# Kernel optimization log

Hardware: AMD Instinct MI355X
Metric: run time of the kernel (lower is better)

The kernel has to match this reference:

```python
import jax, jax.numpy as jnp
import numpy as np

DIM = 512
NUM_LATENTS = 512
HIDDEN = 48  # PointEmbed sinusoidal embedding dim (divisible by 6)


def make_basis():
    k = HIDDEN // 6
    e = (2.0 ** np.arange(k)) * np.pi
    z = np.zeros(k)
    basis = np.stack([
        np.concatenate([e, z, z]),
        np.concatenate([z, e, z]),
        np.concatenate([z, z, e]),
    ])  # [3, HIDDEN//2]
    return jnp.asarray(basis, jnp.float32)


def layernorm(x, g, b, eps=1e-5):
    m = x.mean(-1, keepdims=True)
    v = ((x - m) ** 2).mean(-1, keepdims=True)
    return (x - m) / jnp.sqrt(v + eps) * g + b


def point_embed(x, basis, w, b):
    # x: [B, N, 3] -> [B, N, DIM//2]
    proj = jnp.einsum('bnd,de->bne', x, basis)
    feat = jnp.concatenate([jnp.sin(proj), jnp.cos(proj), x], axis=-1)  # [B,N,51]
    return feat @ w + b


def fps_single(points, num_samples):
    # deterministic farthest point sampling starting at index 0; non-differentiable
    pts = jax.lax.stop_gradient(points)
    N = pts.shape[0]

    def body(carry, _):
        dists, last = carry
        d = jnp.sum((pts - pts[last]) ** 2, axis=-1)
        dists = jnp.minimum(dists, d)
        nxt = jnp.argmax(dists).astype(jnp.int32)
        return (dists, nxt), nxt

    init = (jnp.full((N,), 1e10, pts.dtype), jnp.int32(0))
    _, idxs = jax.lax.scan(body, init, None, length=num_samples - 1)
    return jnp.concatenate([jnp.zeros((1,), jnp.int32), idxs])


def setup_inputs() -> dict:
    key = jax.random.key(0)
    ks = jax.random.split(key, 16)
    B, T, N, D = 16, 3, 2048, 3
    s = 0.02
    inp = {
        'pc': jax.random.normal(ks[0], (B, T, N, D), jnp.float32),
        'pc2': jax.random.normal(ks[1], (B, T, N, D), jnp.float32),
        'basis': make_basis(),
        'pe_w': jax.random.normal(ks[2], (HIDDEN + 3, DIM // 2), jnp.float32) * s,
        'pe_b': jnp.zeros((DIM // 2,), jnp.float32),
        'lnq_g': jnp.ones((DIM,), jnp.float32), 'lnq_b': jnp.zeros((DIM,), jnp.float32),
        'lnc_g': jnp.ones((DIM,), jnp.float32), 'lnc_b': jnp.zeros((DIM,), jnp.float32),
        'wq': jax.random.normal(ks[3], (DIM, DIM), jnp.float32) * s,
        'wkv': jax.random.normal(ks[4], (DIM, 2 * DIM), jnp.float32) * s,
        'wo': jax.random.normal(ks[5], (DIM, DIM), jnp.float32) * s,
        'bo': jnp.zeros((DIM,), jnp.float32),
        'lnf_g': jnp.ones((DIM,), jnp.float32), 'lnf_b': jnp.zeros((DIM,), jnp.float32),
        'w1': jax.random.normal(ks[6], (DIM, 8 * DIM), jnp.float32) * s,
        'b1': jnp.zeros((8 * DIM,), jnp.float32),
        'w2': jax.random.normal(ks[7], (4 * DIM, DIM), jnp.float32) * s,
        'b2': jnp.zeros((DIM,), jnp.float32),
    }
    return inp


def reference(pc, pc2, basis, pe_w, pe_b, lnq_g, lnq_b, lnc_g, lnc_b,
              wq, wkv, wo, bo, lnf_g, lnf_b, w1, b1, w2, b2):
    B, T, N, D = pc.shape
    # FPS on the first frame, per batch element (batch-local indices)
    idx = jax.vmap(lambda p: fps_single(p, NUM_LATENTS))(pc[:, 0])  # [B, M]
    idx4 = idx[:, None, :, None]  # broadcast over T and D
    sampled = jnp.take_along_axis(pc, idx4, axis=2).reshape(B * T, NUM_LATENTS, D)
    sampled2 = jnp.take_along_axis(pc2, idx4, axis=2).reshape(B * T, NUM_LATENTS, D)
    pcf = pc.reshape(B * T, N, D)
    pcf2 = pc2.reshape(B * T, N, D)

    emb_s = jnp.concatenate([point_embed(sampled, basis, pe_w, pe_b),
                             point_embed(sampled2, basis, pe_w, pe_b)], axis=-1)
    emb_c = jnp.concatenate([point_embed(pcf, basis, pe_w, pe_b),
                             point_embed(pcf2, basis, pe_w, pe_b)], axis=-1)

    # PreNorm cross-attention (1 head, dim_head = DIM)
    q_in = layernorm(emb_s, lnq_g, lnq_b)
    c_in = layernorm(emb_c, lnc_g, lnc_b)
    q = q_in @ wq
    kv = c_in @ wkv
    k, v = jnp.split(kv, 2, axis=-1)
    scale = DIM ** -0.5
    attn = jax.nn.softmax(jnp.einsum('bmd,bnd->bmn', q, k) * scale, axis=-1)
    out = jnp.einsum('bmn,bnd->bmd', attn, v) @ wo + bo
    x = out + emb_s

    # PreNorm GEGLU feed-forward
    h = layernorm(x, lnf_g, lnf_b) @ w1 + b1
    a, g = jnp.split(h, 2, axis=-1)
    x = (a * jax.nn.gelu(g, approximate=False)) @ w2 + b2 + x

    return x.reshape(B, T, NUM_LATENTS, DIM)
```

## Files before the change

### kernel.cpp

```cpp
#include <hip/hip_runtime.h>

#define NB    16
#define NT    3
#define NCTX  2048
#define NLAT  512
#define DIMV  512
#define HALFD 256
#define NFEAT 51
#define NBT   48
#define MROWS 24576
#define GRP   6
#define NGRP  8
#define GROWS 12288
#define FUSED_BLKS (NB + GROWS/16 + 4096)

typedef unsigned short bfu;
typedef short bf16x8 __attribute__((ext_vector_type(8)));
typedef float f32x4  __attribute__((ext_vector_type(4)));
typedef float f32x2  __attribute__((ext_vector_type(2)));

__device__ __forceinline__ float bf2f(bfu u){ return __uint_as_float(((unsigned int)u) << 16); }
__device__ __forceinline__ bfu f2bf(float f){
  unsigned int u = __float_as_uint(f);
  u += 0x7FFFu + ((u >> 16) & 1u);
  return (bfu)(u >> 16);
}
__device__ __forceinline__ float loadE(const float* p){ return *p; }
__device__ __forceinline__ float loadE(const bfu* p){ return bf2f(*p); }
__device__ __forceinline__ void storeE(float* p, float v){ *p = v; }
__device__ __forceinline__ void storeE(bfu* p, float v){ *p = f2bf(v); }
__device__ __forceinline__ bfu to_bfu(float f){ return f2bf(f); }
__device__ __forceinline__ bfu to_bfu(bfu u){ return u; }

#define GLD16(gp, lp) __builtin_amdgcn_global_load_lds(                       \
    (const __attribute__((address_space(1))) unsigned int*)(gp),              \
    (__attribute__((address_space(3))) unsigned int*)(lp), 16, 0, 0)

template<int KSTEP>
__device__ __forceinline__ int swzr(int r){
  constexpr int CPR = KSTEP / 8;
  return (KSTEP == 32) ? ((r >> 1) & 3) : (r & (CPR - 1));
}

#define DPP_ARGMAX_STAGE(CTRL)                                                \
  {                                                                           \
    const int svb = __builtin_amdgcn_update_dpp(vb, vb, CTRL, 0xF, 0xF, false); \
    const int sib = __builtin_amdgcn_update_dpp(ib, ib, CTRL, 0xF, 0xF, false); \
    const float sv = __int_as_float(svb);                                     \
    const float cv = __int_as_float(vb);                                      \
    if (sv > cv || (sv == cv && sib < ib)){ vb = svb; ib = sib; }             \
  }

__device__ __forceinline__ void fps_body(int b, int tid, const float* __restrict__ pc,
                                         int* __restrict__ idx_out,
                                         float4* pts, int (*mbuf)[8]){
  const int lane = tid & 63, w = tid >> 6;
  const int wbase = w << 9;
  const float* src = pc + (size_t)b * (NT * NCTX * 3);

  f32x2 x2[4], y2[4], z2[4], d2[4];
  #pragma unroll
  for (int j = 0; j < 4; ++j){
    #pragma unroll
    for (int h = 0; h < 2; ++h){
      const int p = wbase + ((2 * j + h) << 6) + lane;
      const float xx = src[p * 3 + 0];
      const float yy = src[p * 3 + 1];
      const float zz = src[p * 3 + 2];
      x2[j][h] = xx; y2[j][h] = yy; z2[j][h] = zz;
      pts[p] = make_float4(xx, yy, zz, 0.f);
    }
    d2[j][0] = 1e10f; d2[j][1] = 1e10f;
  }
  if (tid == 0) idx_out[b * NLAT] = 0;
  __syncthreads();

  int last = 0;
  for (int step = 1; step < NLAT; ++step){
    const float4 lp = pts[last];

    #pragma unroll
    for (int j = 0; j < 4; ++j){
      const f32x2 dx = x2[j] - lp.x;
      const f32x2 dy = y2[j] - lp.y;
      const f32x2 dz = z2[j] - lp.z;
      const f32x2 dd = (dx * dx + dy * dy) + dz * dz;
      f32x2 nd;
      nd[0] = fminf(d2[j][0], dd[0]);
      nd[1] = fminf(d2[j][1], dd[1]);
      d2[j] = nd;
    }

    float av[4]; int as_[4];
    #pragma unroll
    for (int j = 0; j < 4; ++j){
      const float lo = d2[j][0], hi = d2[j][1];
      const bool t = hi > lo;
      av[j]  = t ? hi : lo;
      as_[j] = t ? 2 * j + 1 : 2 * j;
    }
    #pragma unroll
    for (int wdt = 2; wdt; wdt >>= 1){
      #pragma unroll
      for (int j = 0; j < wdt; ++j){
        const float lv = av[2 * j], rv = av[2 * j + 1];
        const int   li = as_[2 * j], ri = as_[2 * j + 1];
        const bool t = rv > lv;
        av[j]  = t ? rv : lv;
        as_[j] = t ? ri : li;
      }
    }

    int vb = __float_as_int(av[0]);
    int ib = wbase + (as_[0] << 6) + lane;
    DPP_ARGMAX_STAGE(0x111)
    DPP_ARGMAX_STAGE(0x112)
    DPP_ARGMAX_STAGE(0x114)
    DPP_ARGMAX_STAGE(0x118)
    DPP_ARGMAX_STAGE(0x142)
    DPP_ARGMAX_STAGE(0x143)

    const int par = step & 1;
    if (lane == 63){ mbuf[par][w * 2] = vb; mbuf[par][w * 2 + 1] = ib; }
    __syncthreads();
    const int4 q0 = *(const int4*)&mbuf[par][0];
    const int4 q1 = *(const int4*)&mbuf[par][4];
    float bv = __int_as_float(q0.x); int bi = q0.y;
    { const float v1 = __int_as_float(q0.z); if (v1 > bv){ bv = v1; bi = q0.w; } }
    { const float v2 = __int_as_float(q1.x); if (v2 > bv){ bv = v2; bi = q1.y; } }
    { const float v3 = __int_as_float(q1.z); if (v3 > bv){ bv = v3; bi = q1.w; } }
    last = bi;
    if (tid == 0) idx_out[b * NLAT + step] = last;
  }
}

template<bool GATHER, bool WRITE_EMB>
__device__ __forceinline__ void embed_body(
    int bid, int tid,
    const float* __restrict__ pc, const float* __restrict__ pc2,
    const int* __restrict__ idx,
    const float* __restrict__ basis, const float* __restrict__ pe_w,
    const float* __restrict__ pe_b,
    const float* __restrict__ ln_g, const float* __restrict__ ln_b,
    bfu* __restrict__ emb, bfu* __restrict__ lnout, int nppbt,
    float (*feat)[16][NFEAT + 1], float (*outb)[DIMV])
{
  const int p0 = bid << 4;

  if (tid < 32){
    const int s = tid >> 4, p = tid & 15;
    const int gp = p0 + p;
    const int bt = gp / nppbt;
    const int n  = gp - bt * nppbt;
    const int bb = bt / NT;
    const int srcn = GATHER ? idx[bb * NLAT + n] : n;
    const float* sp = (s ? pc2 : pc) + ((size_t)bt * NCTX + srcn) * 3;
    feat[s][p][48] = sp[0]; feat[s][p][49] = sp[1]; feat[s][p][50] = sp[2];
  }
  __syncthreads();

  #pragma unroll
  for (int t = 0; t < 3; ++t){
    const int wk  = tid * 3 + t;
    const int spq = wk / 24;
    const int e   = wk - spq * 24;
    const int s = spq >> 4, p = spq & 15;
    const float x0 = feat[s][p][48], x1 = feat[s][p][49], x2 = feat[s][p][50];
    const float pr = __fadd_rn(__fadd_rn(__fmul_rn(x0, basis[e]),
                                         __fmul_rn(x1, basis[24 + e])),
                               __fmul_rn(x2, basis[48 + e]));
    feat[s][p][e]      = sinf(pr);
    feat[s][p][24 + e] = cosf(pr);
  }
  __syncthreads();

  {
    float w[NFEAT];
    #pragma unroll
    for (int k = 0; k < NFEAT; ++k) w[k] = pe_w[k * HALFD + tid];
    const float bv = pe_b[tid];
    #pragma unroll
    for (int half = 0; half < 2; ++half){
      for (int p = 0; p < 16; ++p){
        float acc = bv;
        #pragma unroll
        for (int k = 0; k < NFEAT; ++k) acc = fmaf(feat[half][p][k], w[k], acc);
        outb[p][half * HALFD + tid] = acc;
      }
    }
  }
  __syncthreads();

  const int lane = tid & 63, wv = tid >> 6;
  for (int pp = 0; pp < 4; ++pp){
    const int p = (wv << 2) + pp;
    const size_t gp = (size_t)p0 + p;
    float x[8];
    #pragma unroll
    for (int j = 0; j < 8; ++j) x[j] = outb[p][lane + (j << 6)];
    float s = 0.f;
    #pragma unroll
    for (int j = 0; j < 8; ++j) s += x[j];
    for (int o = 32; o; o >>= 1) s += __shfl_xor(s, o, 64);
    const float m = s * (1.0f / 512.0f);
    float s2 = 0.f;
    #pragma unroll
    for (int j = 0; j < 8; ++j){ const float d = x[j] - m; s2 = fmaf(d, d, s2); }
    for (int o = 32; o; o >>= 1) s2 += __shfl_xor(s2, o, 64);
    const float inv = 1.0f / sqrtf(s2 * (1.0f / 512.0f) + 1e-5f);
    #pragma unroll
    for (int j = 0; j < 8; ++j){
      const int c = lane + (j << 6);
      const float r = (x[j] - m) * inv * ln_g[c] + ln_b[c];
      const size_t o2 = gp * DIMV + c;
      if (WRITE_EMB) emb[o2] = f2bf(x[j]);
      lnout[o2] = f2bf(r);
    }
  }
}

template<bool GATHER, bool WRITE_EMB>
__global__ __launch_bounds__(256) void embed_kernel(
    const float* __restrict__ pc, const float* __restrict__ pc2,
    const int* __restrict__ idx,
    const float* __restrict__ basis, const float* __restrict__ pe_w,
    const float* __restrict__ pe_b,
    const float* __restrict__ ln_g, const float* __restrict__ ln_b,
    bfu* __restrict__ emb, bfu* __restrict__ lnout, int nppbt)
{
  __shared__ float feat[2][16][NFEAT + 1];
  __shared__ float outb[16][DIMV];
  embed_body<GATHER, WRITE_EMB>(blockIdx.x, threadIdx.x, pc, pc2, idx, basis,
      pe_w, pe_b, ln_g, ln_b, emb, lnout, nppbt, feat, outb);
}

template<typename TIN>
__device__ __forceinline__ void transp_body(
    const TIN* __restrict__ in, bfu* __restrict__ out, int R, int C,
    int bx, int by, bfu (*t)[33])
{
  const int c0 = bx * 32, r0 = by * 32;
  const int tx = threadIdx.x & 31, ty = threadIdx.x >> 5;
  #pragma unroll
  for (int rr = ty; rr < 32; rr += 8)
    t[rr][tx] = to_bfu(in[(size_t)(r0 + rr) * C + c0 + tx]);
  __syncthreads();
  #pragma unroll
  for (int rr = ty; rr < 32; rr += 8)
    out[(size_t)(c0 + rr) * R + r0 + tx] = t[tx][rr];
}

__global__ __attribute__((amdgpu_waves_per_eu(1, 1)))
__launch_bounds__(256) void fused_pre(
    const float* __restrict__ pc, const float* __restrict__ pc2,
    int* __restrict__ idx_out,
    const float* __restrict__ basis, const float* __restrict__ pe_w,
    const float* __restrict__ pe_b,
    const float* __restrict__ lnc_g, const float* __restrict__ lnc_b,
    bfu* __restrict__ c_grp,
    const float* __restrict__ wq, const float* __restrict__ wkv,
    const float* __restrict__ wo, const float* __restrict__ w1,
    const float* __restrict__ w2,
    bfu* __restrict__ wqT, bfu* __restrict__ wkvT, bfu* __restrict__ woT,
    bfu* __restrict__ w1T, bfu* __restrict__ w2T)
{
  __shared__ __align__(16) char smem[39424];
  const int bid = blockIdx.x, tid = threadIdx.x;

  if (bid < NB){
    #pragma clang fp contract(off)
    float4* pts = (float4*)smem;
    int (*mbuf)[8] = (int(*)[8])(smem + 32768);
    fps_body(bid, tid, pc, idx_out, pts, mbuf);
    return;
  }
  const int rb = bid - NB;
  if (rb < GROWS / 16){
    embed_body<false, false>(rb, tid, pc, pc2, nullptr, basis, pe_w, pe_b,
                             lnc_g, lnc_b, nullptr, c_grp, NCTX,
                             (float(*)[16][NFEAT + 1])smem,
                             (float(*)[DIMV])(smem + 6656));
    return;
  }
  int tb = rb - GROWS / 16;
  bfu (*tile)[33] = (bfu(*)[33])smem;
  if (tb < 256){ transp_body<float>(wq,  wqT,  512,  512, tb & 15,  tb >> 4, tile); return; }
  tb -= 256;
  if (tb < 512){ transp_body<float>(wkv, wkvT, 512, 1024, tb & 31,  tb >> 5, tile); return; }
  tb -= 512;
  if (tb < 256){ transp_body<float>(wo,  woT,  512,  512, tb & 15,  tb >> 4, tile); return; }
  tb -= 256;
  if (tb < 2048){ transp_body<float>(w1, w1T,  512, 4096, tb & 127, tb >> 7, tile); return; }
  tb -= 2048;
  transp_body<float>(w2, w2T, 2048, 512, tb & 15, tb >> 4, tile);
}

#define EPI_NONE     0
#define EPI_SPLIT    1
#define EPI_SCALE    2
#define EPI_BIAS_RES 3

template<int FH, int KSTEP, typename TC, typename TR, int EPI>
__global__ __launch_bounds__(256, 2) void gemm_mfma(
    const bfu* __restrict__ A, const bfu* __restrict__ B,
    TC* __restrict__ C, TC* __restrict__ C2,
    const float* __restrict__ bias, const TR* __restrict__ res,
    float scale, int N, int K, int lda, int ldb, int ldc,
    long long sA, long long sB, long long sC)
{
  constexpr int BT  = FH * 32;
  constexpr int CPR = KSTEP / 8;
  constexpr int NI  = (BT * CPR) / 256;
  const int bz = blockIdx.z;
  A += (size_t)bz * sA;
  B += (size_t)bz * sB;
  const size_t coff = (size_t)bz * sC;

  __shared__ __align__(16) short As[BT * KSTEP];
  __shared__ __align__(16) short Bs[BT * KSTEP];

  const int tid = threadIdx.x;
  const int lane = tid & 63, w = tid >> 6;
  const int wl = (w << 6) + lane;
  const int m0 = blockIdx.y * BT, n0 = blockIdx.x * BT;
  const int wm = (w & 1) * (FH * 16), wn = (w >> 1) * (FH * 16);
  const int fr = lane & 15, quad = lane >> 4;

  f32x4 acc[FH][FH];
  #pragma unroll
  for (int i = 0; i < FH; ++i)
    #pragma unroll
    for (int j = 0; j < FH; ++j)
      #pragma unroll
      for (int r = 0; r < 4; ++r) acc[i][j][r] = 0.f;

  for (int k0 = 0; k0 < K; k0 += KSTEP){
    #pragma unroll
    for (int i = 0; i < NI; ++i){
      const int ch = i * 256 + wl;
      const int r  = ch / CPR, cs = ch & (CPR - 1);
      const int cg = cs ^ swzr<KSTEP>(r);
      short* la = (short*)As + ((i * 256 + (w << 6)) << 3);
      short* lb = (short*)Bs + ((i * 256 + (w << 6)) << 3);
      GLD16(A + (size_t)(m0 + r) * lda + k0 + cg * 8, la);
      GLD16(B + (size_t)(n0 + r) * ldb + k0 + cg * 8, lb);
    }
    __syncthreads();
    #pragma unroll
    for (int kk = 0; kk < KSTEP / 32; ++kk){
      bf16x8 af[FH], bf[FH];
      #pragma unroll
      for (int i = 0; i < FH; ++i){
        const int row = wm + i * 16 + fr;
        const int cl = (kk * 4 + quad) ^ swzr<KSTEP>(row);
        af[i] = *(const bf16x8*)&As[row * KSTEP + (cl << 3)];
      }
      #pragma unroll
      for (int j = 0; j < FH; ++j){
        const int row = wn + j * 16 + fr;
        const int cl = (kk * 4 + quad) ^ swzr<KSTEP>(row);
        bf[j] = *(const bf16x8*)&Bs[row * KSTEP + (cl << 3)];
      }
      #pragma unroll
      for (int i = 0; i < FH; ++i)
        #pragma unroll
        for (int j = 0; j < FH; ++j)
          acc[i][j] = __builtin_amdgcn_mfma_f32_16x16x32_bf16(af[i], bf[j], acc[i][j], 0, 0, 0);
    }
    __syncthreads();
  }

  TC* Cp = C + coff;
  #pragma unroll
  for (int i = 0; i < FH; ++i){
    #pragma unroll
    for (int r = 0; r < 4; ++r){
      const int cm = m0 + wm + i * 16 + quad * 4 + r;
      #pragma unroll
      for (int j = 0; j < FH; ++j){
        const int cn = n0 + wn + j * 16 + fr;
        float v = acc[i][j][r];
        if (EPI == EPI_SCALE)    v *= scale;
        if (EPI == EPI_BIAS_RES) v = v + bias[cn] + loadE(&res[coff + (size_t)cm * ldc + cn]);
        if (EPI == EPI_SPLIT){
          const int half = N >> 1;
          if (cn < half) storeE(&C [(size_t)cm * half + cn],          v);
          else           storeE(&C2[(size_t)cm * half + (cn - half)], v);
        } else {
          storeE(&Cp[(size_t)cm * ldc + cn], v);
        }
      }
    }
  }
}

__global__ __launch_bounds__(256, 1) void mlp1_mfma(
    const bfu* __restrict__ A, const bfu* __restrict__ B,
    const float* __restrict__ b1, bfu* __restrict__ act)
{
  constexpr int KSTEP = 64, CPR = 8, NI = 4;
  __shared__ __align__(16) short As[128 * KSTEP];
  __shared__ __align__(16) short Ba[128 * KSTEP];
  __shared__ __align__(16) short Bg[128 * KSTEP];

  const int tid = threadIdx.x;
  const int lane = tid & 63, w = tid >> 6;
  const int wl = (w << 6) + lane;
  const int m0 = blockIdx.y * 128, n0 = blockIdx.x * 128;
  const int wm = (w & 1) * 64, wn = (w >> 1) * 64;
  const int fr = lane & 15, quad = lane >> 4;

  f32x4 acca[4][4], accg[4][4];
  #pragma unroll
  for (int i = 0; i < 4; ++i)
    #pragma unroll
    for (int j = 0; j < 4; ++j)
      #pragma unroll
      for (int r = 0; r < 4; ++r){ acca[i][j][r] = 0.f; accg[i][j][r] = 0.f; }

  for (int k0 = 0; k0 < 512; k0 += KSTEP){
    #pragma unroll
    for (int i = 0; i < NI; ++i){
      const int ch = i * 256 + wl;
      const int r  = ch / CPR, cs = ch & (CPR - 1);
      const int cg = cs ^ swzr<KSTEP>(r);
      short* da = (short*)As + ((i * 256 + (w << 6)) << 3);
      short* db = (short*)Ba + ((i * 256 + (w << 6)) << 3);
      short* dg = (short*)Bg + ((i * 256 + (w << 6)) << 3);
      GLD16(A + (size_t)(m0 + r) * 512 + k0 + cg * 8, da);
      GLD16(B + (size_t)(n0 + r) * 512 + k0 + cg * 8, db);
      GLD16(B + (size_t)(n0 + 2048 + r) * 512 + k0 + cg * 8, dg);
    }
    __syncthreads();
    #pragma unroll
    for (int kk = 0; kk < KSTEP / 32; ++kk){
      bf16x8 af[4], ba[4], bg[4];
      #pragma unroll
      for (int i = 0; i < 4; ++i){
        const int row = wm + i * 16 + fr;
        const int cl = (kk * 4 + quad) ^ swzr<KSTEP>(row);
        af[i] = *(const bf16x8*)&As[row * KSTEP + (cl << 3)];
      }
      #pragma unroll
      for (int j = 0; j < 4; ++j){
        const int row = wn + j * 16 + fr;
        const int cl = (kk * 4 + quad) ^ swzr<KSTEP>(row);
        ba[j] = *(const bf16x8*)&Ba[row * KSTEP + (cl << 3)];
        bg[j] = *(const bf16x8*)&Bg[row * KSTEP + (cl << 3)];
      }
      #pragma unroll
      for (int i = 0; i < 4; ++i)
        #pragma unroll
        for (int j = 0; j < 4; ++j){
          acca[i][j] = __builtin_amdgcn_mfma_f32_16x16x32_bf16(af[i], ba[j], acca[i][j], 0, 0, 0);
          accg[i][j] = __builtin_amdgcn_mfma_f32_16x16x32_bf16(af[i], bg[j], accg[i][j], 0, 0, 0);
        }
    }
    __syncthreads();
  }

  #pragma unroll
  for (int i = 0; i < 4; ++i){
    #pragma unroll
    for (int r = 0; r < 4; ++r){
      const int cm = m0 + wm + i * 16 + quad * 4 + r;
      #pragma unroll
      for (int j = 0; j < 4; ++j){
        const int cn = n0 + wn + j * 16 + fr;
        const float a = acca[i][j][r] + b1[cn];
        const float g = accg[i][j][r] + b1[cn + 2048];
        const float ge = g * 0.5f * (1.0f + erff(g * 0.70710678118654752f));
        act[(size_t)cm * 2048 + cn] = f2bf(a * ge);
      }
    }
  }
}

__global__ __launch_bounds__(256) void softmax_kernel(bfu* __restrict__ sc){
  __shared__ float red[4];
  const int tid = threadIdx.x;
  const int lane = tid & 63, wv = tid >> 6;
  bfu* rp = sc + (size_t)blockIdx.x * NCTX;
  float x[8];
  #pragma unroll
  for (int j = 0; j < 8; ++j) x[j] = bf2f(rp[tid + (j << 8)]);
  float mx = x[0];
  #pragma unroll
  for (int j = 1; j < 8; ++j) mx = fmaxf(mx, x[j]);
  for (int o = 32; o; o >>= 1) mx = fmaxf(mx, __shfl_xor(mx, o, 64));
  if (lane == 0) red[wv] = mx;
  __syncthreads();
  mx = fmaxf(fmaxf(red[0], red[1]), fmaxf(red[2], red[3]));
  float sum = 0.f;
  #pragma unroll
  for (int j = 0; j < 8; ++j){ x[j] = __expf(x[j] - mx); sum += x[j]; }
  for (int o = 32; o; o >>= 1) sum += __shfl_xor(sum, o, 64);
  __syncthreads();
  if (lane == 0) red[wv] = sum;
  __syncthreads();
  sum = red[0] + red[1] + red[2] + red[3];
  const float inv = 1.0f / sum;
  #pragma unroll
  for (int j = 0; j < 8; ++j) rp[tid + (j << 8)] = f2bf(x[j] * inv);
}

__global__ __launch_bounds__(256) void ln_kernel(const float* __restrict__ in,
                                                 const float* __restrict__ g,
                                                 const float* __restrict__ b,
                                                 bfu* __restrict__ out){
  const int tid = threadIdx.x, lane = tid & 63, wv = tid >> 6;
  const size_t row = (size_t)blockIdx.x * 4 + wv;
  const float* rp = in + row * DIMV;
  float x[8];
  #pragma unroll
  for (int j = 0; j < 8; ++j) x[j] = rp[lane + (j << 6)];
  float s = 0.f;
  #pragma unroll
  for (int j = 0; j < 8; ++j) s += x[j];
  for (int o = 32; o; o >>= 1) s += __shfl_xor(s, o, 64);
  const float m = s * (1.0f / 512.0f);
  float s2 = 0.f;
  #pragma unroll
  for (int j = 0; j < 8; ++j){ const float d = x[j] - m; s2 = fmaf(d, d, s2); }
  for (int o = 32; o; o >>= 1) s2 += __shfl_xor(s2, o, 64);
  const float inv = 1.0f / sqrtf(s2 * (1.0f / 512.0f) + 1e-5f);
  bfu* op = out + row * DIMV;
  #pragma unroll
  for (int j = 0; j < 8; ++j){
    const int c = lane + (j << 6);
    op[c] = f2bf((x[j] - m) * inv * g[c] + b[c]);
  }
}

extern "C" void kernel_launch(void* const* d_in, const int* in_sizes, int n_in,
                              void* d_out, int out_size, void* d_ws, size_t ws_size,
                              hipStream_t stream)
{
  (void)in_sizes; (void)n_in; (void)out_size;
  if (ws_size < 121667584ull) return;

  const float* pc    = (const float*)d_in[0];
  const float* pc2   = (const float*)d_in[1];
  const float* basis = (const float*)d_in[2];
  const float* pe_w  = (const float*)d_in[3];
  const float* pe_b  = (const float*)d_in[4];
  const float* lnq_g = (const float*)d_in[5];
  const float* lnq_b = (const float*)d_in[6];
  const float* lnc_g = (const float*)d_in[7];
  const float* lnc_b = (const float*)d_in[8];
  const float* wq    = (const float*)d_in[9];
  const float* wkv   = (const float*)d_in[10];
  const float* wo    = (const float*)d_in[11];
  const float* bo    = (const float*)d_in[12];
  const float* lnf_g = (const float*)d_in[13];
  const float* lnf_b = (const float*)d_in[14];
  const float* w1    = (const float*)d_in[15];
  const float* b1    = (const float*)d_in[16];
  const float* w2    = (const float*)d_in[17];
  const float* b2    = (const float*)d_in[18];
  float* xout = (float*)d_out;

  char* ws = (char*)d_ws;
  int* idxb   = (int*)(ws);
  bfu* emb_s  = (bfu*)(ws + 32768);
  bfu* q_in   = (bfu*)(ws + 25198592);
  bfu* c_grp  = (bfu*)(ws + 50364416);
  bfu* k_grp  = (bfu*)(ws + 62947328);
  bfu* v_grp  = (bfu*)(ws + 75530240);
  bfu* qbuf   = (bfu*)(ws + 88113152);
  bfu* wqT    = (bfu*)(ws + 113278976);
  bfu* wkvT   = (bfu*)(ws + 113803264);
  bfu* woT    = (bfu*)(ws + 114851840);
  bfu* w1T    = (bfu*)(ws + 115376128);
  bfu* w2T    = (bfu*)(ws + 119570432);
  bfu* scores  = c_grp;
  bfu* vT      = v_grp;
  bfu* attnout = q_in;
  bfu* lnx     = qbuf;
  bfu* actb    = emb_s;

  fused_pre<<<FUSED_BLKS, 256, 0, stream>>>(
      pc, pc2, idxb, basis, pe_w, pe_b, lnc_g, lnc_b, c_grp,
      wq, wkv, wo, w1, w2, wqT, wkvT, woT, w1T, w2T);

  embed_kernel<true, true><<<MROWS/16, 256, 0, stream>>>(
      pc, pc2, idxb, basis, pe_w, pe_b, lnq_g, lnq_b, emb_s, q_in, NLAT);

  gemm_mfma<4, 64, bfu, float, EPI_NONE><<<dim3(4, 192, 1), 256, 0, stream>>>(
      q_in, wqT, qbuf, nullptr, nullptr, nullptr, 1.0f,
      512, 512, 512, 512, 512, 0, 0, 0);

  for (int g = 0; g < NGRP; ++g){
    const int bt0 = g * GRP;
    if (g > 0){
      embed_kernel<false, false><<<GROWS/16, 256, 0, stream>>>(
          pc + (size_t)bt0 * NCTX * 3, pc2 + (size_t)bt0 * NCTX * 3, nullptr,
          basis, pe_w, pe_b, lnc_g, lnc_b, nullptr, c_grp, NCTX);
    }

    gemm_mfma<4, 64, bfu, float, EPI_NONE><<<dim3(4, 96, 1), 256, 0, stream>>>(
        c_grp, wkvT, k_grp, nullptr, nullptr, nullptr, 1.0f,
        512, 512, 512, 512, 512, 0, 0, 0);

    gemm_mfma<4, 64, bfu, float, EPI_NONE><<<dim3(16, 4, GRP), 256, 0, stream>>>(
        wkvT + 512 * 512, c_grp, v_grp, nullptr, nullptr, nullptr, 1.0f,
        2048, 512, 512, 512, 2048, 0, 1048576, 1048576);

    gemm_mfma<4, 64, bfu, float, EPI_SCALE><<<dim3(16, 4, GRP), 256, 0, stream>>>(
        qbuf + (size_t)bt0 * 262144, k_grp, scores, nullptr, nullptr, nullptr,
        0.044194173824159216f,
        2048, 512, 512, 512, 2048, 262144, 1048576, 1048576);

    softmax_kernel<<<GRP * 512, 256, 0, stream>>>(scores);

    gemm_mfma<2, 128, bfu, float, EPI_NONE><<<dim3(8, 8, GRP), 256, 0, stream>>>(
        scores, vT, attnout + (size_t)bt0 * 262144, nullptr, nullptr, nullptr, 1.0f,
        512, 2048, 2048, 2048, 512, 1048576, 1048576, 262144);
  }

  gemm_mfma<4, 64, float, bfu, EPI_BIAS_RES><<<dim3(4, 192, 1), 256, 0, stream>>>(
      attnout, woT, xout, nullptr, bo, emb_s, 1.0f,
      512, 512, 512, 512, 512, 0, 0, 0);

  ln_kernel<<<MROWS/4, 256, 0, stream>>>(xout, lnf_g, lnf_b, lnx);

  for (int h = 0; h < 2; ++h){
    const size_t ro = (size_t)h * 12288;
    mlp1_mfma<<<dim3(16, 96, 1), 256, 0, stream>>>(
        lnx + ro * 512, w1T, b1, actb);
    gemm_mfma<4, 64, float, float, EPI_BIAS_RES><<<dim3(4, 96, 1), 256, 0, stream>>>(
        actb, w2T, xout + ro * 512, nullptr, b2, xout + ro * 512, 1.0f,
        512, 2048, 2048, 2048, 512, 0, 0, 0);
  }
}
```

Baseline: 1.527 ms.

## Broadcast FPS winner coordinates via LDS and merge Q/K/V GEMMs into one launch

```diff
diff --git a/kernel.cpp b/kernel.cpp
--- a/kernel.cpp
+++ b/kernel.cpp
@@ -53,7 +53,7 @@
 
 __device__ __forceinline__ void fps_body(int b, int tid, const float* __restrict__ pc,
                                          int* __restrict__ idx_out,
-                                         float4* pts, int (*mbuf)[8]){
+                                         float4 (*xyz)[4], int2 (*vi)[4]){
   const int lane = tid & 63, w = tid >> 6;
   const int wbase = w << 9;
   const float* src = pc + (size_t)b * (NT * NCTX * 3);
@@ -64,21 +64,20 @@
     #pragma unroll
     for (int h = 0; h < 2; ++h){
       const int p = wbase + ((2 * j + h) << 6) + lane;
-      const float xx = src[p * 3 + 0];
-      const float yy = src[p * 3 + 1];
-      const float zz = src[p * 3 + 2];
-      x2[j][h] = xx; y2[j][h] = yy; z2[j][h] = zz;
-      pts[p] = make_float4(xx, yy, zz, 0.f);
+      x2[j][h] = src[p * 3 + 0];
+      y2[j][h] = src[p * 3 + 1];
+      z2[j][h] = src[p * 3 + 2];
     }
     d2[j][0] = 1e10f; d2[j][1] = 1e10f;
   }
-  if (tid == 0) idx_out[b * NLAT] = 0;
+  if (tid == 0){
+    idx_out[b * NLAT] = 0;
+    xyz[0][0] = make_float4(x2[0][0], y2[0][0], z2[0][0], 0.f);
+  }
   __syncthreads();
-
-  int last = 0;
+  float4 lp = xyz[0][0];
+
   for (int step = 1; step < NLAT; ++step){
-    const float4 lp = pts[last];
-
     #pragma unroll
     for (int j = 0; j < 4; ++j){
       const f32x2 dx = x2[j] - lp.x;
@@ -121,16 +120,41 @@
     DPP_ARGMAX_STAGE(0x143)
 
     const int par = step & 1;
-    if (lane == 63){ mbuf[par][w * 2] = vb; mbuf[par][w * 2 + 1] = ib; }
+    if (lane == 63) vi[par][w] = make_int2(vb, ib);
+    if ((ib & 63) == lane){
+      const int s = (ib >> 6) & 7;
+      const bool b0 = (s & 1) != 0, b1 = (s & 2) != 0, b2 = (s & 4) != 0;
+      const float xa = b0 ? x2[0][1] : x2[0][0];
+      const float xb = b0 ? x2[1][1] : x2[1][0];
+      const float xc = b0 ? x2[2][1] : x2[2][0];
+      const float xd = b0 ? x2[3][1] : x2[3][0];
+      const float ya = b0 ? y2[0][1] : y2[0][0];
+      const float yb = b0 ? y2[1][1] : y2[1][0];
+      const float yc = b0 ? y2[2][1] : y2[2][0];
+      const float yd = b0 ? y2[3][1] : y2[3][0];
+      const float za = b0 ? z2[0][1] : z2[0][0];
+      const float zb = b0 ? z2[1][1] : z2[1][0];
+      const float zc = b0 ? z2[2][1] : z2[2][0];
+      const float zd = b0 ? z2[3][1] : z2[3][0];
+      const float xe = b1 ? xb : xa, xf = b1 ? xd : xc;
+      const float ye = b1 ? yb : ya, yf = b1 ? yd : yc;
+      const float ze = b1 ? zb : za, zf = b1 ? zd : zc;
+      xyz[par][w] = make_float4(b2 ? xf : xe, b2 ? yf : ye, b2 ? zf : ze, 0.f);
+    }
     __syncthreads();
-    const int4 q0 = *(const int4*)&mbuf[par][0];
-    const int4 q1 = *(const int4*)&mbuf[par][4];
-    float bv = __int_as_float(q0.x); int bi = q0.y;
-    { const float v1 = __int_as_float(q0.z); if (v1 > bv){ bv = v1; bi = q0.w; } }
-    { const float v2 = __int_as_float(q1.x); if (v2 > bv){ bv = v2; bi = q1.y; } }
-    { const float v3 = __int_as_float(q1.z); if (v3 > bv){ bv = v3; bi = q1.w; } }
-    last = bi;
-    if (tid == 0) idx_out[b * NLAT + step] = last;
+
+    const int2 r0 = vi[par][0], r1 = vi[par][1], r2 = vi[par][2], r3 = vi[par][3];
+    const float4 c0 = xyz[par][0], c1 = xyz[par][1], c2 = xyz[par][2], c3 = xyz[par][3];
+    float bv = __int_as_float(r0.x); int bi = r0.y;
+    float bx = c0.x, by = c0.y, bz = c0.z;
+    { const float v1 = __int_as_float(r1.x);
+      if (v1 > bv){ bv = v1; bi = r1.y; bx = c1.x; by = c1.y; bz = c1.z; } }
+    { const float v2 = __int_as_float(r2.x);
+      if (v2 > bv){ bv = v2; bi = r2.y; bx = c2.x; by = c2.y; bz = c2.z; } }
+    { const float v3 = __int_as_float(r3.x);
+      if (v3 > bv){ bv = v3; bi = r3.y; bx = c3.x; by = c3.y; bz = c3.z; } }
+    lp = make_float4(bx, by, bz, 0.f);
+    if (tid == 0) idx_out[b * NLAT + step] = bi;
   }
 }
 
@@ -269,9 +293,9 @@
 
   if (bid < NB){
     #pragma clang fp contract(off)
-    float4* pts = (float4*)smem;
-    int (*mbuf)[8] = (int(*)[8])(smem + 32768);
-    fps_body(bid, tid, pc, idx_out, pts, mbuf);
+    float4 (*xyz)[4] = (float4(*)[4])smem;
+    int2   (*vi)[4]  = (int2(*)[4])(smem + 128);
+    fps_body(bid, tid, pc, idx_out, xyz, vi);
     return;
   }
   const int rb = bid - NB;
@@ -389,6 +413,101 @@
         } else {
           storeE(&Cp[(size_t)cm * ldc + cn], v);
         }
+      }
+    }
+  }
+}
+
+__global__ __launch_bounds__(256, 2) void kv_mfma(
+    int nq,
+    const bfu* __restrict__ qA, const bfu* __restrict__ qB, bfu* __restrict__ qC,
+    const bfu* __restrict__ cg, const bfu* __restrict__ wkvT,
+    bfu* __restrict__ kg, bfu* __restrict__ vg)
+{
+  constexpr int KSTEP = 64, CPR = 8, NI = 4;
+  const bfu *A, *B; bfu *C; int m0, n0, ldc;
+  {
+    int bid = blockIdx.x;
+    if (bid < nq){
+      A = qA; B = qB; C = qC;
+      m0 = (bid >> 2) * 128; n0 = (bid & 3) * 128; ldc = 512;
+    } else {
+      bid -= nq;
+      if (bid < 384){
+        A = cg; B = wkvT; C = kg;
+        m0 = (bid >> 2) * 128; n0 = (bid & 3) * 128; ldc = 512;
+      } else {
+        const int r = bid - 384, z = r >> 6, rr = r & 63;
+        A = wkvT + 512 * 512;
+        B = cg + (size_t)z * 1048576;
+        C = vg + (size_t)z * 1048576;
+        m0 = (rr >> 4) * 128; n0 = (rr & 15) * 128; ldc = 2048;
+      }
+    }
+  }
+
+  __shared__ __align__(16) short As[128 * KSTEP];
+  __shared__ __align__(16) short Bs[128 * KSTEP];
+
+  const int tid = threadIdx.x;
+  const int lane = tid & 63, w = tid >> 6;
+  const int wl = (w << 6) + lane;
+  const int wm = (w & 1) * 64, wn = (w >> 1) * 64;
+  const int fr = lane & 15, quad = lane >> 4;
+
+  f32x4 acc[4][4];
+  #pragma unroll
+  for (int i = 0; i < 4; ++i)
+    #pragma unroll
+    for (int j = 0; j < 4; ++j)
+      #pragma unroll
+      for (int r = 0; r < 4; ++r) acc[i][j][r] = 0.f;
+
+  for (int k0 = 0; k0 < 512; k0 += KSTEP){
+    #pragma unroll
+    for (int i = 0; i < NI; ++i){
+      const int ch = i * 256 + wl;
+      const int r  = ch / CPR, cs = ch & (CPR - 1);
+      const int cg2 = cs ^ swzr<KSTEP>(r);
+      short* la = (short*)As + ((i * 256 + (w << 6)) << 3);
+      short* lb = (short*)Bs + ((i * 256 + (w << 6)) << 3);
+      GLD16(A + (size_t)(m0 + r) * 512 + k0 + cg2 * 8, la);
+      GLD16(B + (size_t)(n0 + r) * 512 + k0 + cg2 * 8, lb);
+    }
+    __syncthreads();
+    #pragma unroll
+    for (int kk = 0; kk < KSTEP / 32; ++kk){
+      bf16x8 af[4], bf[4];
+      #pragma unroll
+      for (int i = 0; i < 4; ++i){
+        const int row = wm + i * 16 + fr;
+        const int cl = (kk * 4 + quad) ^ swzr<KSTEP>(row);
+        af[i] = *(const bf16x8*)&As[row * KSTEP + (cl << 3)];
+      }
+      #pragma unroll
+      for (int j = 0; j < 4; ++j){
+        const int row = wn + j * 16 + fr;
+        const int cl = (kk * 4 + quad) ^ swzr<KSTEP>(row);
+        bf[j] = *(const bf16x8*)&Bs[row * KSTEP + (cl << 3)];
+      }
+      #pragma unroll
+      for (int i = 0; i < 4; ++i)
+        #pragma unroll
+        for (int j = 0; j < 4; ++j)
+          acc[i][j] = __builtin_amdgcn_mfma_f32_16x16x32_bf16(af[i], bf[j], acc[i][j], 0, 0, 0);
+    }
+    __syncthreads();
+  }
+
+  #pragma unroll
+  for (int i = 0; i < 4; ++i){
+    #pragma unroll
+    for (int r = 0; r < 4; ++r){
+      const int cm = m0 + wm + i * 16 + quad * 4 + r;
+      #pragma unroll
+      for (int j = 0; j < 4; ++j){
+        const int cn = n0 + wn + j * 16 + fr;
+        C[(size_t)cm * ldc + cn] = f2bf(acc[i][j][r]);
       }
     }
   }
@@ -586,10 +705,6 @@
   embed_kernel<true, true><<<MROWS/16, 256, 0, stream>>>(
       pc, pc2, idxb, basis, pe_w, pe_b, lnq_g, lnq_b, emb_s, q_in, NLAT);
 
-  gemm_mfma<4, 64, bfu, float, EPI_NONE><<<dim3(4, 192, 1), 256, 0, stream>>>(
-      q_in, wqT, qbuf, nullptr, nullptr, nullptr, 1.0f,
-      512, 512, 512, 512, 512, 0, 0, 0);
-
   for (int g = 0; g < NGRP; ++g){
     const int bt0 = g * GRP;
     if (g > 0){
@@ -598,13 +713,9 @@
           basis, pe_w, pe_b, lnc_g, lnc_b, nullptr, c_grp, NCTX);
     }
 
-    gemm_mfma<4, 64, bfu, float, EPI_NONE><<<dim3(4, 96, 1), 256, 0, stream>>>(
-        c_grp, wkvT, k_grp, nullptr, nullptr, nullptr, 1.0f,
-        512, 512, 512, 512, 512, 0, 0, 0);
-
-    gemm_mfma<4, 64, bfu, float, EPI_NONE><<<dim3(16, 4, GRP), 256, 0, stream>>>(
-        wkvT + 512 * 512, c_grp, v_grp, nullptr, nullptr, nullptr, 1.0f,
-        2048, 512, 512, 512, 2048, 0, 1048576, 1048576);
+    const int nq = (g == 0) ? 768 : 0;
+    kv_mfma<<<nq + 768, 256, 0, stream>>>(
+        nq, q_in, wqT, qbuf, c_grp, wkvT, k_grp, v_grp);
 
     gemm_mfma<4, 64, bfu, float, EPI_SCALE><<<dim3(16, 4, GRP), 256, 0, stream>>>(
         qbuf + (size_t)bt0 * 262144, k_grp, scores, nullptr, nullptr, nullptr,
```

Measured after the change: 1.652 ms. 1.08x slower.
